# Optimization experiments

Hardware: AMD Instinct MI355X
Metric: run time of the kernel (lower is better)

The kernel has to match this reference:

```python
import jax, jax.numpy as jnp
import numpy as np

D = 1024      # model_dim
H = 16        # num_heads
HD = D // H   # head_size
B = 4
S = 2048


def setup_inputs() -> dict:
    key = jax.random.key(0)
    ks = jax.random.split(key, 6)
    sc = 1.0 / np.sqrt(D)
    embedded = jax.random.normal(ks[0], (B, S, D), dtype=jnp.float32)
    # Per-head projection weights stacked: [H, D, HD] (nn.Linear, bias=False)
    Wq = jax.random.normal(ks[1], (H, D, HD), dtype=jnp.float32) * sc
    Wk = jax.random.normal(ks[2], (H, D, HD), dtype=jnp.float32) * sc
    Wv = jax.random.normal(ks[3], (H, D, HD), dtype=jnp.float32) * sc
    # Output projection nn.Linear(D, D) with bias
    Wo = jax.random.normal(ks[4], (D, D), dtype=jnp.float32) * sc
    bo = jax.random.normal(ks[5], (D,), dtype=jnp.float32) * sc
    return {"embedded": embedded, "Wq": Wq, "Wk": Wk, "Wv": Wv, "Wo": Wo, "bo": bo}


def reference(embedded, Wq, Wk, Wv, Wo, bo):
    # q,k,v: [B, H, S, HD]
    q = jnp.einsum('bsd,hde->bhse', embedded, Wq)
    k = jnp.einsum('bsd,hde->bhse', embedded, Wk)
    v = jnp.einsum('bsd,hde->bhse', embedded, Wv)
    scores = jnp.einsum('bhse,bhte->bhst', q, k) / jnp.sqrt(jnp.float32(HD))
    causal = jnp.tril(jnp.ones((S, S), dtype=bool))  # [S, S]
    scores = jnp.where(causal, scores, -jnp.inf)
    attn = jax.nn.softmax(scores, axis=-1)
    ctx = jnp.einsum('bhst,bhte->bhse', attn, v)  # [B, H, S, HD]
    # concat heads -> [B, S, D]
    concat = jnp.transpose(ctx, (0, 2, 1, 3)).reshape(B, S, D)
    # dropout=0.0 -> identity
    return concat @ Wo.T + bo
```

## Files before the change

kernel.cpp:

```cpp
#include <hip/hip_runtime.h>
#include <hip/hip_bf16.h>
#include <stdint.h>
#include <stddef.h>

typedef __bf16 bf16;
typedef __bf16 bf16x8 __attribute__((ext_vector_type(8)));
typedef float f32x4 __attribute__((ext_vector_type(4)));
typedef float f32x16 __attribute__((ext_vector_type(16)));


__device__ __forceinline__ void gload16(const void* g, void* lds) {
  __builtin_amdgcn_global_load_lds(
      (const __attribute__((address_space(1))) unsigned int*)(uintptr_t)g,
      (__attribute__((address_space(3))) unsigned int*)(unsigned int)(uintptr_t)lds,
      16, 0, 0);
}

__device__ __forceinline__ bf16x8 lds_read8(const bf16* base, int row, int slot) {
  const char* p = (const char*)base + row * 128 + ((slot ^ (row & 7)) << 4);
  return *(const bf16x8*)p;
}


__global__ void k_cvt_embed(const float* __restrict__ src, bf16* __restrict__ dst) {
  int i = blockIdx.x * blockDim.x + threadIdx.x;
  const float4* s4 = (const float4*)src;
  float4 a = s4[2 * i], b = s4[2 * i + 1];
  bf16x8 v;
  v[0] = (bf16)a.x; v[1] = (bf16)a.y; v[2] = (bf16)a.z; v[3] = (bf16)a.w;
  v[4] = (bf16)b.x; v[5] = (bf16)b.y; v[6] = (bf16)b.z; v[7] = (bf16)b.w;
  ((bf16x8*)dst)[i] = v;
}


__global__ void k_cvt_w(const float* __restrict__ Wq, const float* __restrict__ Wk,
                        const float* __restrict__ Wv, const float* __restrict__ Wo,
                        bf16* __restrict__ WT, bf16* __restrict__ WoB) {
  int i = blockIdx.x * blockDim.x + threadIdx.x;
  if (i < 16 * 192 * 1024) {
    int h = i / (192 * 1024);
    int rem = i - h * (192 * 1024);
    int r = rem >> 10;
    int d = rem & 1023;
    const float* W = (r < 64) ? Wq : (r < 128 ? Wk : Wv);
    int e = r & 63;
    WT[i] = (bf16)W[h * 65536 + d * 64 + e];
  } else {
    int j = i - 16 * 192 * 1024;
    WoB[j] = (bf16)Wo[j];
  }
}


__launch_bounds__(256, 2)
__global__ void k_qkv(const bf16* __restrict__ E, const bf16* __restrict__ WT,
                      bf16* __restrict__ Qo, bf16* __restrict__ Ko, bf16* __restrict__ Vo) {
  __shared__ __align__(16) bf16 As[128 * 64];
  __shared__ __align__(16) bf16 Bs[192 * 64];
  const int h = blockIdx.y;
  const int m0 = blockIdx.x * 128;
  const int tid = threadIdx.x;
  const int w = tid >> 6, lane = tid & 63;
  const int wm = w >> 1, wn = w & 1;
  const int cl = lane & 15, g4 = lane >> 4;
  const int srow = lane >> 3;
  const int scol = ((lane & 7) ^ (lane >> 3)) << 3;
  const bf16* Wh = WT + (size_t)h * 192 * 1024;
  f32x4 zero = {0.f, 0.f, 0.f, 0.f};
  f32x4 acc[4][6];
#pragma unroll
  for (int m = 0; m < 4; ++m)
#pragma unroll
    for (int n = 0; n < 6; ++n) acc[m][n] = zero;

  for (int kt = 0; kt < 16; ++kt) {
    const int k0 = kt * 64;
    __syncthreads();
#pragma unroll
    for (int c = 0; c < 4; ++c) {
      int cc = w * 4 + c;
      gload16(E + (size_t)(m0 + cc * 8 + srow) * 1024 + k0 + scol, (char*)As + cc * 1024);
    }
#pragma unroll
    for (int c = 0; c < 6; ++c) {
      int cc = w * 6 + c;
      gload16(Wh + (size_t)(cc * 8 + srow) * 1024 + k0 + scol, (char*)Bs + cc * 1024);
    }
    __syncthreads();
#pragma unroll
    for (int kk = 0; kk < 2; ++kk) {
      bf16x8 a[4], b[6];
#pragma unroll
      for (int m = 0; m < 4; ++m) a[m] = lds_read8(As, wm * 64 + m * 16 + cl, kk * 4 + g4);
#pragma unroll
      for (int n = 0; n < 6; ++n) b[n] = lds_read8(Bs, wn * 96 + n * 16 + cl, kk * 4 + g4);
#pragma unroll
      for (int m = 0; m < 4; ++m)
#pragma unroll
        for (int n = 0; n < 6; ++n)
          acc[m][n] = __builtin_amdgcn_mfma_f32_16x16x32_bf16(a[m], b[n], acc[m][n], 0, 0, 0);
    }
  }
#pragma unroll
  for (int n = 0; n < 6; ++n) {
    int ncol = wn * 96 + n * 16 + cl;
    int which = ncol >> 6, e = ncol & 63;
    bf16* dst = which == 0 ? Qo : (which == 1 ? Ko : Vo);
    const float sc = (which == 0) ? 0.18033688f : 1.0f;
#pragma unroll
    for (int m = 0; m < 4; ++m) {
#pragma unroll
      for (int r = 0; r < 4; ++r) {
        int row = m0 + wm * 64 + m * 16 + g4 * 4 + r;
        int bb = row >> 11, ss = row & 2047;
        dst[(((size_t)(bb * 16 + h) * 2048 + ss) << 6) + e] = (bf16)(acc[m][n][r] * sc);
      }
    }
  }
}


__launch_bounds__(512)
__global__ void k_attn(const bf16* __restrict__ Qg, const bf16* __restrict__ Kg,
                       const bf16* __restrict__ Vg, bf16* __restrict__ CTX) {
  __shared__ __align__(16) bf16 KS[2][8192];
  __shared__ __align__(16) bf16 VT[2][2][4096];
  const int b = blockIdx.x;
  const int bh = b & 63;
  const int g = b >> 6;
  const int qt = (g < 4) ? g : 11 - g;
  const int q0 = qt * 256;
  const int tid = threadIdx.x, w = tid >> 6, lane = tid & 63;
  const int ql = lane & 31, hi = lane >> 5;
  const int q = q0 + 32 * w + ql;
  const int qmin = q0 + 32 * w;
  const int qmax = qmin + 31;
  const bf16* Qb = Qg + (size_t)bh * (2048 * 64);
  const bf16* Kb = Kg + (size_t)bh * (2048 * 64);
  const bf16* Vb = Vg + (size_t)bh * (2048 * 64);
  const int ntk = 2 * qt + 2;

  bf16x8 qf[4];
#pragma unroll
  for (int ks = 0; ks < 4; ++ks)
    qf[ks] = *(const bf16x8*)(Qb + (size_t)q * 64 + ks * 16 + hi * 8);

  f32x16 o0, o1;
#pragma unroll
  for (int i = 0; i < 16; ++i) { o0[i] = 0.f; o1[i] = 0.f; }
  float mr = -1e30f, ls = 0.f;

  const int srowK = w * 8 + (lane >> 3);
  const int scolK = ((lane & 7) ^ ((lane >> 3) & 7)) << 3;
  const int lanep = (lane & ~12) | ((lane & 4) << 1) | ((lane & 8) >> 1);
  int offs[4];
#pragma unroll
  for (int ks = 0; ks < 4; ++ks) offs[ks] = (ks * 32 + hi * 16) ^ ((ql & 7) << 4);

  auto do_half = [&](int kv0h, const char* kbase, const char* vbase) {
    float p[32];
    f32x16 s0, s1;
#pragma unroll
    for (int i = 0; i < 16; ++i) { s0[i] = 0.f; s1[i] = 0.f; }
    __builtin_amdgcn_s_setprio(1);
#pragma unroll
    for (int ks = 0; ks < 4; ++ks) {
      bf16x8 k0 = *(const bf16x8*)(kbase + ql * 128 + offs[ks]);
      bf16x8 k1 = *(const bf16x8*)(kbase + (32 + ql) * 128 + offs[ks]);
      s0 = __builtin_amdgcn_mfma_f32_32x32x16_bf16(k0, qf[ks], s0, 0, 0, 0);
      s1 = __builtin_amdgcn_mfma_f32_32x32x16_bf16(k1, qf[ks], s1, 0, 0, 0);
    }
    __builtin_amdgcn_s_setprio(0);
#pragma unroll
    for (int r = 0; r < 16; ++r) { p[r] = s0[r]; p[16 + r] = s1[r]; }
    if (kv0h + 63 > qmin) {
#pragma unroll
      for (int kb = 0; kb < 2; ++kb)
#pragma unroll
        for (int r = 0; r < 16; ++r) {
          int key = kv0h + kb * 32 + (r & 3) + 8 * (r >> 2) + 4 * hi;
          if (key > q) p[kb * 16 + r] = -1e30f;
        }
    }
    float t8[8];
#pragma unroll
    for (int i = 0; i < 8; ++i)
      t8[i] = fmaxf(fmaxf(fmaxf(p[i], p[i + 8]), p[i + 16]), p[i + 24]);
    float mA = fmaxf(fmaxf(t8[0], t8[1]), fmaxf(t8[2], t8[3]));
    float mB = fmaxf(fmaxf(t8[4], t8[5]), fmaxf(t8[6], t8[7]));
    float pmax = fmaxf(mA, mB);
    pmax = fmaxf(pmax, __shfl_xor(pmax, 32));
    if (__any(pmax - mr > 8.0f)) {
      float mnew = fmaxf(mr, pmax);
      float al = exp2f(mr - mnew);
      mr = mnew; ls *= al;
#pragma unroll
      for (int i = 0; i < 16; ++i) { o0[i] *= al; o1[i] *= al; }
    }
#pragma unroll
    for (int i = 0; i < 32; ++i) p[i] = exp2f(p[i] - mr);
    float a8[8];
#pragma unroll
    for (int i = 0; i < 8; ++i) a8[i] = (p[i] + p[i + 8]) + (p[i + 16] + p[i + 24]);
    float rs = (a8[0] + a8[1]) + (a8[2] + a8[3]) + (a8[4] + a8[5]) + (a8[6] + a8[7]);
    rs += __shfl_xor(rs, 32);
    ls += rs;
    __builtin_amdgcn_s_setprio(1);
#pragma unroll
    for (int ks = 0; ks < 4; ++ks) {
      bf16x8 pf;
#pragma unroll
      for (int j = 0; j < 8; ++j) pf[j] = (bf16)p[ks * 8 + j];
      bf16x8 v0 = *(const bf16x8*)(vbase + ql * 128 + offs[ks]);
      bf16x8 v1 = *(const bf16x8*)(vbase + (32 + ql) * 128 + offs[ks]);
      o0 = __builtin_amdgcn_mfma_f32_32x32x16_bf16(v0, pf, o0, 0, 0, 0);
      o1 = __builtin_amdgcn_mfma_f32_32x32x16_bf16(v1, pf, o1, 0, 0, 0);
    }
    __builtin_amdgcn_s_setprio(0);
  };

  {
    gload16(Kb + (size_t)srowK * 64 + scolK, (char*)KS[0] + w * 1024);
    gload16(Kb + (size_t)(64 + srowK) * 64 + scolK, (char*)KS[0] + 8192 + w * 1024);
    bf16x8 v0 = *(const bf16x8*)(Vb + (size_t)lane * 64 + w * 8);
    bf16x8 v1 = *(const bf16x8*)(Vb + (size_t)(64 + lane) * 64 + w * 8);
#pragma unroll
    for (int j = 0; j < 8; ++j) {
      *(bf16*)((char*)VT[0][0] + w * 1024 + j * 128 + ((lanep * 2) ^ (j << 4))) = v0[j];
      *(bf16*)((char*)VT[0][1] + w * 1024 + j * 128 + ((lanep * 2) ^ (j << 4))) = v1[j];
    }
  }

  int cur = 0;
  for (int t = 0; t < ntk; ++t) {
    const int kv0 = t * 128;
    __syncthreads();
    bf16x8 vn0, vn1;
    const bool more = (t + 1 < ntk);
    if (more) {
      const int kn = kv0 + 128;
      vn0 = *(const bf16x8*)(Vb + (size_t)(kn + lane) * 64 + w * 8);
      vn1 = *(const bf16x8*)(Vb + (size_t)(kn + 64 + lane) * 64 + w * 8);
      gload16(Kb + (size_t)(kn + srowK) * 64 + scolK, (char*)KS[cur ^ 1] + w * 1024);
      gload16(Kb + (size_t)(kn + 64 + srowK) * 64 + scolK, (char*)KS[cur ^ 1] + 8192 + w * 1024);
    }
    if (kv0 <= qmax)
      do_half(kv0, (const char*)KS[cur], (const char*)VT[cur][0]);
    if (more) {
#pragma unroll
      for (int j = 0; j < 8; ++j) {
        *(bf16*)((char*)VT[cur ^ 1][0] + w * 1024 + j * 128 + ((lanep * 2) ^ (j << 4))) = vn0[j];
        *(bf16*)((char*)VT[cur ^ 1][1] + w * 1024 + j * 128 + ((lanep * 2) ^ (j << 4))) = vn1[j];
      }
    }
    if (kv0 + 64 <= qmax)
      do_half(kv0 + 64, (const char*)KS[cur] + 8192, (const char*)VT[cur][1]);
    cur ^= 1;
  }

  const float inv = 1.0f / ls;
  const int bb = bh >> 4, hh = bh & 15;
  bf16* Cp = CTX + ((size_t)(bb * 2048 + q) * 1024) + hh * 64;
#pragma unroll
  for (int r = 0; r < 16; ++r) {
    int d0 = (r & 3) + 8 * (r >> 2) + 4 * hi;
    Cp[d0] = (bf16)(o0[r] * inv);
    Cp[32 + d0] = (bf16)(o1[r] * inv);
  }
}


__launch_bounds__(256, 2)
__global__ void k_oproj(const bf16* __restrict__ X, const bf16* __restrict__ Wb,
                        const float* __restrict__ bo, float* __restrict__ out) {
  __shared__ __align__(16) bf16 As[128 * 64];
  __shared__ __align__(16) bf16 Bs[128 * 64];
  const int m0 = blockIdx.x * 128, n0 = blockIdx.y * 128;
  const int tid = threadIdx.x, w = tid >> 6, lane = tid & 63;
  const int wm = w >> 1, wn = w & 1;
  const int cl = lane & 15, g4 = lane >> 4;
  const int srow = lane >> 3;
  const int scol = ((lane & 7) ^ (lane >> 3)) << 3;
  f32x4 zero = {0.f, 0.f, 0.f, 0.f};
  f32x4 acc[4][4];
#pragma unroll
  for (int m = 0; m < 4; ++m)
#pragma unroll
    for (int n = 0; n < 4; ++n) acc[m][n] = zero;

  for (int kt = 0; kt < 16; ++kt) {
    const int k0 = kt * 64;
    __syncthreads();
#pragma unroll
    for (int c = 0; c < 4; ++c) {
      int cc = w * 4 + c;
      gload16(X + (size_t)(m0 + cc * 8 + srow) * 1024 + k0 + scol, (char*)As + cc * 1024);
      gload16(Wb + (size_t)(n0 + cc * 8 + srow) * 1024 + k0 + scol, (char*)Bs + cc * 1024);
    }
    __syncthreads();
#pragma unroll
    for (int kk = 0; kk < 2; ++kk) {
      bf16x8 a[4], b[4];
#pragma unroll
      for (int m = 0; m < 4; ++m) a[m] = lds_read8(As, wm * 64 + m * 16 + cl, kk * 4 + g4);
#pragma unroll
      for (int n = 0; n < 4; ++n) b[n] = lds_read8(Bs, wn * 64 + n * 16 + cl, kk * 4 + g4);
#pragma unroll
      for (int m = 0; m < 4; ++m)
#pragma unroll
        for (int n = 0; n < 4; ++n)
          acc[m][n] = __builtin_amdgcn_mfma_f32_16x16x32_bf16(a[m], b[n], acc[m][n], 0, 0, 0);
    }
  }
#pragma unroll
  for (int n = 0; n < 4; ++n) {
    int col = n0 + wn * 64 + n * 16 + cl;
    float bias = bo[col];
#pragma unroll
    for (int m = 0; m < 4; ++m)
#pragma unroll
      for (int r = 0; r < 4; ++r) {
        int row = m0 + wm * 64 + m * 16 + g4 * 4 + r;
        out[(size_t)row * 1024 + col] = acc[m][n][r] + bias;
      }
  }
}


extern "C" void kernel_launch(void* const* d_in, const int* in_sizes, int n_in,
                              void* d_out, int out_size, void* d_ws, size_t ws_size,
                              hipStream_t stream) {
  const float* emb = (const float*)d_in[0];
  const float* Wq  = (const float*)d_in[1];
  const float* Wk  = (const float*)d_in[2];
  const float* Wv  = (const float*)d_in[3];
  const float* Wo  = (const float*)d_in[4];
  const float* bo  = (const float*)d_in[5];
  float* out = (float*)d_out;

  const size_t NEED = (size_t)72 << 20;
  if (ws_size < NEED) return;

  char* ws = (char*)d_ws;
  bf16* E   = (bf16*)(ws);
  bf16* WT  = (bf16*)(ws + ((size_t)16 << 20));
  bf16* WoB = (bf16*)(ws + ((size_t)22 << 20));
  bf16* Qw  = (bf16*)(ws + ((size_t)24 << 20));
  bf16* Kw  = (bf16*)(ws + ((size_t)40 << 20));
  bf16* Vw  = (bf16*)(ws + ((size_t)56 << 20));
  bf16* CTX = E;

  k_cvt_embed<<<4096, 256, 0, stream>>>(emb, E);
  k_cvt_w<<<16384, 256, 0, stream>>>(Wq, Wk, Wv, Wo, WT, WoB);
  k_qkv<<<dim3(64, 16), 256, 0, stream>>>(E, WT, Qw, Kw, Vw);
  k_attn<<<512, 512, 0, stream>>>(Qw, Kw, Vw, CTX);
  k_oproj<<<dim3(64, 8), 256, 0, stream>>>(CTX, WoB, bo, out);
}
```

Baseline: 179.9 us.

## Split attention half-step into QK/softmax/PV stages and interleave across halves

Splits the per-64-key processing into separate QK^T, softmax and PV lambdas and reorders them so the second half's QK^T MFMAs are issued before the first half's PV, letting matrix work overlap softmax math. It also simplifies the causal mask comparison and the max-reduction tree using 3-input max, and works on the accumulators in place instead of copying them to a temp array. The launch bounds now request 4 waves per EU, which caps registers and risks spills now that two score tiles are live at once.

```diff
diff --git a/kernel.cpp b/kernel.cpp
--- a/kernel.cpp
+++ b/kernel.cpp
@@ -19,6 +19,10 @@
 __device__ __forceinline__ bf16x8 lds_read8(const bf16* base, int row, int slot) {
   const char* p = (const char*)base + row * 128 + ((slot ^ (row & 7)) << 4);
   return *(const bf16x8*)p;
+}
+
+__device__ __forceinline__ float f3max(float a, float b, float c) {
+  return fmaxf(fmaxf(a, b), c);
 }
 
 
@@ -120,7 +124,7 @@
 }
 
 
-__launch_bounds__(512)
+__launch_bounds__(512, 4)
 __global__ void k_attn(const bf16* __restrict__ Qg, const bf16* __restrict__ Kg,
                        const bf16* __restrict__ Vg, bf16* __restrict__ CTX) {
   __shared__ __align__(16) bf16 KS[2][8192];
@@ -157,9 +161,7 @@
 #pragma unroll
   for (int ks = 0; ks < 4; ++ks) offs[ks] = (ks * 32 + hi * 16) ^ ((ql & 7) << 4);
 
-  auto do_half = [&](int kv0h, const char* kbase, const char* vbase) {
-    float p[32];
-    f32x16 s0, s1;
+  auto QKT = [&](const char* kbase, f32x16& s0, f32x16& s1) {
 #pragma unroll
     for (int i = 0; i < 16; ++i) { s0[i] = 0.f; s1[i] = 0.f; }
     __builtin_amdgcn_s_setprio(1);
@@ -171,24 +173,34 @@
       s1 = __builtin_amdgcn_mfma_f32_32x32x16_bf16(k1, qf[ks], s1, 0, 0, 0);
     }
     __builtin_amdgcn_s_setprio(0);
-#pragma unroll
-    for (int r = 0; r < 16; ++r) { p[r] = s0[r]; p[16 + r] = s1[r]; }
+  };
+
+  auto SM = [&](int kv0h, f32x16& s0, f32x16& s1, bf16x8* pf) {
     if (kv0h + 63 > qmin) {
-#pragma unroll
-      for (int kb = 0; kb < 2; ++kb)
-#pragma unroll
-        for (int r = 0; r < 16; ++r) {
-          int key = kv0h + kb * 32 + (r & 3) + 8 * (r >> 2) + 4 * hi;
-          if (key > q) p[kb * 16 + r] = -1e30f;
-        }
-    }
-    float t8[8];
-#pragma unroll
-    for (int i = 0; i < 8; ++i)
-      t8[i] = fmaxf(fmaxf(fmaxf(p[i], p[i + 8]), p[i + 16]), p[i + 24]);
-    float mA = fmaxf(fmaxf(t8[0], t8[1]), fmaxf(t8[2], t8[3]));
-    float mB = fmaxf(fmaxf(t8[4], t8[5]), fmaxf(t8[6], t8[7]));
-    float pmax = fmaxf(mA, mB);
+      int dqh = q - kv0h - 4 * hi;
+#pragma unroll
+      for (int r = 0; r < 16; ++r) {
+        const int c = (r & 3) + 8 * (r >> 2);
+        if (c > dqh) s0[r] = -1e30f;
+        if (c + 32 > dqh) s1[r] = -1e30f;
+      }
+    }
+    float x0 = f3max(s0[0], s0[1], s0[2]);
+    float x1 = f3max(s0[3], s0[4], s0[5]);
+    float x2 = f3max(s0[6], s0[7], s0[8]);
+    float x3 = f3max(s0[9], s0[10], s0[11]);
+    float x4 = f3max(s0[12], s0[13], s0[14]);
+    float x5 = f3max(s0[15], s1[0], s1[1]);
+    float x6 = f3max(s1[2], s1[3], s1[4]);
+    float x7 = f3max(s1[5], s1[6], s1[7]);
+    float x8 = f3max(s1[8], s1[9], s1[10]);
+    float x9 = f3max(s1[11], s1[12], s1[13]);
+    float xa = fmaxf(s1[14], s1[15]);
+    float y0 = f3max(x0, x1, x2);
+    float y1 = f3max(x3, x4, x5);
+    float y2 = f3max(x6, x7, x8);
+    float y3 = fmaxf(x9, xa);
+    float pmax = f3max(y0, y1, fmaxf(y2, y3));
     pmax = fmaxf(pmax, __shfl_xor(pmax, 32));
     if (__any(pmax - mr > 8.0f)) {
       float mnew = fmaxf(mr, pmax);
@@ -198,23 +210,33 @@
       for (int i = 0; i < 16; ++i) { o0[i] *= al; o1[i] *= al; }
     }
 #pragma unroll
-    for (int i = 0; i < 32; ++i) p[i] = exp2f(p[i] - mr);
+    for (int i = 0; i < 16; ++i) {
+      s0[i] = exp2f(s0[i] - mr);
+      s1[i] = exp2f(s1[i] - mr);
+    }
     float a8[8];
 #pragma unroll
-    for (int i = 0; i < 8; ++i) a8[i] = (p[i] + p[i + 8]) + (p[i + 16] + p[i + 24]);
-    float rs = (a8[0] + a8[1]) + (a8[2] + a8[3]) + (a8[4] + a8[5]) + (a8[6] + a8[7]);
+    for (int i = 0; i < 8; ++i) a8[i] = (s0[i] + s0[i + 8]) + (s1[i] + s1[i + 8]);
+    float rs = ((a8[0] + a8[1]) + (a8[2] + a8[3])) + ((a8[4] + a8[5]) + (a8[6] + a8[7]));
     rs += __shfl_xor(rs, 32);
     ls += rs;
+#pragma unroll
+    for (int j = 0; j < 8; ++j) {
+      pf[0][j] = (bf16)s0[j];
+      pf[1][j] = (bf16)s0[8 + j];
+      pf[2][j] = (bf16)s1[j];
+      pf[3][j] = (bf16)s1[8 + j];
+    }
+  };
+
+  auto PV = [&](const char* vbase, const bf16x8* pf) {
     __builtin_amdgcn_s_setprio(1);
 #pragma unroll
     for (int ks = 0; ks < 4; ++ks) {
-      bf16x8 pf;
-#pragma unroll
-      for (int j = 0; j < 8; ++j) pf[j] = (bf16)p[ks * 8 + j];
       bf16x8 v0 = *(const bf16x8*)(vbase + ql * 128 + offs[ks]);
       bf16x8 v1 = *(const bf16x8*)(vbase + (32 + ql) * 128 + offs[ks]);
-      o0 = __builtin_amdgcn_mfma_f32_32x32x16_bf16(v0, pf, o0, 0, 0, 0);
-      o1 = __builtin_amdgcn_mfma_f32_32x32x16_bf16(v1, pf, o1, 0, 0, 0);
+      o0 = __builtin_amdgcn_mfma_f32_32x32x16_bf16(v0, pf[ks], o0, 0, 0, 0);
+      o1 = __builtin_amdgcn_mfma_f32_32x32x16_bf16(v1, pf[ks], o1, 0, 0, 0);
     }
     __builtin_amdgcn_s_setprio(0);
   };
@@ -244,8 +266,16 @@
       gload16(Kb + (size_t)(kn + srowK) * 64 + scolK, (char*)KS[cur ^ 1] + w * 1024);
       gload16(Kb + (size_t)(kn + 64 + srowK) * 64 + scolK, (char*)KS[cur ^ 1] + 8192 + w * 1024);
     }
-    if (kv0 <= qmax)
-      do_half(kv0, (const char*)KS[cur], (const char*)VT[cur][0]);
+    const bool act0 = (kv0 <= qmax);
+    const bool act1 = (kv0 + 64 <= qmax);
+    f32x16 sA0, sA1, sB0, sB1;
+    bf16x8 pf0[4], pf1[4];
+    if (act0) {
+      QKT((const char*)KS[cur], sA0, sA1);
+      SM(kv0, sA0, sA1, pf0);
+    }
+    if (act1) QKT((const char*)KS[cur] + 8192, sB0, sB1);
+    if (act0) PV((const char*)VT[cur][0], pf0);
     if (more) {
 #pragma unroll
       for (int j = 0; j < 8; ++j) {
@@ -253,8 +283,10 @@
         *(bf16*)((char*)VT[cur ^ 1][1] + w * 1024 + j * 128 + ((lanep * 2) ^ (j << 4))) = vn1[j];
       }
     }
-    if (kv0 + 64 <= qmax)
-      do_half(kv0 + 64, (const char*)KS[cur] + 8192, (const char*)VT[cur][1]);
+    if (act1) {
+      SM(kv0 + 64, sB0, sB1, pf1);
+      PV((const char*)VT[cur][1], pf1);
+    }
     cur ^= 1;
   }
 
```

Result: slower. 241.3 us (+34.1%).
